# Kernel optimization log

Measured on AMD Instinct MI355X. Metric: run time of the kernel, lower is better.

The kernel has to match this reference:

```python
import jax, jax.numpy as jnp
import numpy as np

H = 50      # hidden_size (fixed in source)
IN = 7      # input_size = len(features)
B = 1024    # batch
T = 512     # seq_len
FC1 = 25
OUT = 1


def setup_inputs() -> dict:
    key = jax.random.key(0)
    ks = jax.random.split(key, 24)
    s = 1.0 / np.sqrt(H)  # PyTorch LSTM/Linear default uniform init scale

    def u(k, shape):
        return jax.random.uniform(k, shape, jnp.float32, -s, s)

    d = {"x": jax.random.normal(ks[0], (B, T, IN), jnp.float32)}
    # 4 stacked LSTM layers total: lstm1 has 2 layers (in=7 then 50), lstm2 has 2 layers (in=50)
    in_sizes = [IN, H, H, H]
    for l, isz in enumerate(in_sizes):
        d[f"Wih{l}"] = u(ks[1 + 4 * l], (4 * H, isz))
        d[f"Whh{l}"] = u(ks[2 + 4 * l], (4 * H, H))
        d[f"bih{l}"] = u(ks[3 + 4 * l], (4 * H,))
        d[f"bhh{l}"] = u(ks[4 + 4 * l], (4 * H,))
    d["W1"] = u(ks[17], (FC1, H))
    d["b1"] = u(ks[18], (FC1,))
    d["W2"] = u(ks[19], (OUT, FC1))
    d["b2"] = u(ks[20], (OUT,))
    return d


def _lstm_layer(x, Wih, Whh, bih, bhh):
    # x: [B, T, in] -> hidden sequence [B, T, H]. PyTorch gate order: i, f, g, o.
    b, t, _ = x.shape
    h = Whh.shape[1]
    # Precompute input projection for all timesteps in one big GEMM: [T, B, 4H]
    xp = jnp.einsum('bti,gi->tbg', x, Wih) + (bih + bhh)

    def step(carry, xt):
        hs, cs = carry
        gates = xt + hs @ Whh.T                      # [B, 4H]
        i, f, g, o = jnp.split(gates, 4, axis=-1)
        i = jax.nn.sigmoid(i)
        f = jax.nn.sigmoid(f)
        g = jnp.tanh(g)
        o = jax.nn.sigmoid(o)
        cs = f * cs + i * g
        hs = o * jnp.tanh(cs)
        return (hs, cs), hs

    h0 = jnp.zeros((b, h), x.dtype)
    _, hseq = jax.lax.scan(step, (h0, h0), xp)       # hseq: [T, B, H]
    return hseq.transpose(1, 0, 2)


def reference(x, Wih0, Whh0, bih0, bhh0, Wih1, Whh1, bih1, bhh1,
              Wih2, Whh2, bih2, bhh2, Wih3, Whh3, bih3, bhh3,
              W1, b1, W2, b2):
    out = x
    layers = [(Wih0, Whh0, bih0, bhh0), (Wih1, Whh1, bih1, bhh1),
              (Wih2, Whh2, bih2, bhh2), (Wih3, Whh3, bih3, bhh3)]
    for Wih, Whh, bih, bhh in layers:
        out = _lstm_layer(out, Wih, Whh, bih, bhh)
    h = out[:, -1, :]                                # last timestep [B, H]
    # dropout is identity in eval mode
    h = jax.nn.relu(h @ W1.T + b1)
    return h @ W2.T + b2                             # [B, 1]
```

## Files before the change

### kernel.cpp

```cpp
#include <hip/hip_runtime.h>


#define H 50
#define INSZ 7
#define TT 512
#define NL 4
#define FC1N 25
#define BPG 4
#define NBLK 256
#define NTHREADS 1024
#define HS 80
#define BIASL 56

typedef _Float16 half_t;
typedef __attribute__((ext_vector_type(8))) _Float16 half8_t;
typedef __attribute__((ext_vector_type(4))) float float4_t;

struct Params {
  const float* x;
  const float* Wih[NL];
  const float* Whh[NL];
  const float* bih[NL];
  const float* bhh[NL];
  const float* W1;
  const float* b1;
  const float* W2;
  const float* b2;
  float* out;
};

#define MFMA16(A, B, C) __builtin_amdgcn_mfma_f32_16x16x32_f16((A), (B), (C), 0, 0, 0)
#define EXP2F(x) __builtin_amdgcn_exp2f(x)
#define RCPF(x) __builtin_amdgcn_rcpf(x)

__global__ __launch_bounds__(NTHREADS, 4) void lstm_r8(Params p) {
  __shared__ __align__(16) half_t Xpack[2][BPG][HS];
  __shared__ __align__(16) half_t Hbuf[3][2][BPG][HS];
  __shared__ __align__(16) half_t Xstage[64][BPG][8];
  __shared__ float fc_h[BPG][H];
  __shared__ float fc1_buf[BPG][FC1N];

  const int tid = threadIdx.x;
  const int b0 = blockIdx.x * BPG;
  const int lane = tid & 63;
  const int quad = lane >> 4;
  const int col = lane & 15;
  const int glay = tid >> 8;
  const int wl = (((tid >> 6) & 3) + glay) & 3;

  half8_t afrag[4][4];
#pragma unroll
  for (int t4 = 0; t4 < 4; ++t4) {
#pragma unroll
    for (int g = 0; g < 4; ++g) {
      half8_t v;
#pragma unroll
      for (int j = 0; j < 8; ++j) {
        const int r = wl * 64 + t4 * 16 + col;
        const int u = r >> 2, q = r & 3;
        const int k = g * 32 + quad * 8 + j;
        float wv = 0.0f;
        if (u < H) {
          const int row = q * H + u;
          if (glay == 0) {
            if (k < INSZ) wv = p.Wih[0][row * INSZ + k];
            else if (k == 7) wv = p.bih[0][row] + p.bhh[0][row];
            else if (k >= 8 && k < 8 + H) wv = p.Whh[0][row * H + (k - 8)];
          } else if (glay == 1) {
            if (k == 7) wv = p.bih[1][row] + p.bhh[1][row];
            else if (k >= 8 && k < 8 + H) wv = p.Wih[1][row * H + (k - 8)];
            else if (k >= 64 && k < 64 + H) wv = p.Whh[1][row * H + (k - 64)];
          } else {
            if (k < H) wv = p.Wih[glay][row * H + k];
            else if (k == BIASL) wv = p.bih[glay][row] + p.bhh[glay][row];
            else if (k >= 64 && k < 64 + H) wv = p.Whh[glay][row * H + (k - 64)];
          }
        }
        v[j] = (half_t)wv;
      }
      afrag[t4][g] = v;
    }
  }

  {
    unsigned* xz = (unsigned*)Xpack;
    for (int i = tid; i < 2 * BPG * HS / 2; i += NTHREADS) xz[i] = 0u;
    unsigned* hz = (unsigned*)Hbuf;
    for (int i = tid; i < 3 * 2 * BPG * HS / 2; i += NTHREADS) hz[i] = 0u;
  }
  __syncthreads();
  if (tid < 8) {
    Xpack[tid >> 2][tid & 3][7] = (half_t)1.0f;
  } else if (tid < 8 + 24) {
    const int i = tid - 8, l = i >> 3, pr = (i >> 2) & 1, b = i & 3;
    Hbuf[l][pr][b][BIASL] = (half_t)1.0f;
  }
  for (int i = tid; i < 64 * BPG * INSZ; i += NTHREADS) {
    const int t = i / (BPG * INSZ), rem = i % (BPG * INSZ);
    const int b = rem / INSZ, k = rem % INSZ;
    const half_t xh = (half_t)p.x[((size_t)(b0 + b) * TT + t) * INSZ + k];
    Xstage[t][b][k] = xh;
    if (t == 0) Xpack[0][b][k] = xh;
  }
  __syncthreads();

  const int bb = col & 3;
  const int tsel = col >> 2;
  const int uu = 16 * wl + 4 * tsel + quad;
  const bool updact = (uu < H);

  const half_t* pin2[2];
  const half_t* pown2[2];
  half_t* pst2[2];
  if (glay == 0) {
    pin2[0] = &Xpack[0][bb][quad * 8];
    pin2[1] = &Xpack[1][bb][quad * 8];
    pown2[0] = pin2[0];
    pown2[1] = pin2[1];
    pst2[0] = &Xpack[1][bb][8 + uu];
    pst2[1] = &Xpack[0][bb][8 + uu];
  } else if (glay == 1) {
    pin2[0] = &Xpack[0][bb][quad * 8];
    pin2[1] = &Xpack[1][bb][quad * 8];
    pown2[0] = &Hbuf[0][0][bb][quad * 8];
    pown2[1] = &Hbuf[0][1][bb][quad * 8];
    pst2[0] = &Hbuf[0][1][bb][uu];
    pst2[1] = &Hbuf[0][0][bb][uu];
  } else {
    pin2[0] = &Hbuf[glay - 2][0][bb][quad * 8];
    pin2[1] = &Hbuf[glay - 2][1][bb][quad * 8];
    pown2[0] = &Hbuf[glay - 1][0][bb][quad * 8];
    pown2[1] = &Hbuf[glay - 1][1][bb][quad * 8];
    pst2[0] = &Hbuf[glay - 1][1][bb][uu];
    pst2[1] = &Hbuf[glay - 1][0][bb][uu];
  }
  const half_t* in_e = pin2[0];
  const half_t* in_o = pin2[1];
  const half_t* own_e = pown2[0];
  const half_t* own_o = pown2[1];
  half_t* st_e = pst2[0];
  half_t* st_o = pst2[1];

  const bool xwave = (glay == 0) && (wl == 3);
  const bool xcopy = xwave && (lane < BPG * INSZ);
  const int cb = lane / INSZ, ck = lane % INSZ;
  const int rb = lane >> 5;
  const int rt = lane & 31;

  float cst = 0.0f;
  const float4_t fzc = {0.0f, 0.0f, 0.0f, 0.0f};

#define TICK_BODY(PIN, POWN, PST, FCW)                                          \
  {                                                                             \
    float4_t a0 = fzc, a1 = fzc, a2 = fzc, a3 = fzc;                            \
    if (glay == 0) {                                                            \
      const half8_t v0 = *(const half8_t*)(PIN);                                \
      const half8_t v1 = *(const half8_t*)((PIN) + 32);                         \
      if (wl != 3) {                                                            \
        a0 = MFMA16(afrag[0][0], v0, a0); a1 = MFMA16(afrag[1][0], v0, a1);     \
        a2 = MFMA16(afrag[2][0], v0, a2); a3 = MFMA16(afrag[3][0], v0, a3);     \
        a0 = MFMA16(afrag[0][1], v1, a0); a1 = MFMA16(afrag[1][1], v1, a1);     \
        a2 = MFMA16(afrag[2][1], v1, a2); a3 = MFMA16(afrag[3][1], v1, a3);     \
      } else {                                                                  \
        a0 = MFMA16(afrag[0][0], v0, a0);                                       \
        a0 = MFMA16(afrag[0][1], v1, a0);                                       \
      }                                                                         \
    } else {                                                                    \
      const half8_t v0 = *(const half8_t*)(PIN);                                \
      const half8_t v1 = *(const half8_t*)((PIN) + 32);                         \
      const half8_t v2 = *(const half8_t*)(POWN);                               \
      const half8_t v3 = *(const half8_t*)((POWN) + 32);                        \
      if (wl != 3) {                                                            \
        a0 = MFMA16(afrag[0][0], v0, a0); a1 = MFMA16(afrag[1][0], v0, a1);     \
        a2 = MFMA16(afrag[2][0], v0, a2); a3 = MFMA16(afrag[3][0], v0, a3);     \
        a0 = MFMA16(afrag[0][1], v1, a0); a1 = MFMA16(afrag[1][1], v1, a1);     \
        a2 = MFMA16(afrag[2][1], v1, a2); a3 = MFMA16(afrag[3][1], v1, a3);     \
        a0 = MFMA16(afrag[0][2], v2, a0); a1 = MFMA16(afrag[1][2], v2, a1);     \
        a2 = MFMA16(afrag[2][2], v2, a2); a3 = MFMA16(afrag[3][2], v2, a3);     \
        a0 = MFMA16(afrag[0][3], v3, a0); a1 = MFMA16(afrag[1][3], v3, a1);     \
        a2 = MFMA16(afrag[2][3], v3, a2); a3 = MFMA16(afrag[3][3], v3, a3);     \
      } else {                                                                  \
        a0 = MFMA16(afrag[0][0], v0, a0);                                       \
        a0 = MFMA16(afrag[0][1], v1, a0);                                       \
        a0 = MFMA16(afrag[0][2], v2, a0);                                       \
        a0 = MFMA16(afrag[0][3], v3, a0);                                       \
      }                                                                         \
    }                                                                           \
    if (updact) {                                                               \
      const float4_t g01 = (col & 4) ? a1 : a0;                                 \
      const float4_t g23 = (col & 4) ? a3 : a2;                                 \
      const float4_t ga = (col & 8) ? g23 : g01;                                \
      const float di = 1.0f + EXP2F(-1.442695041f * ga[0]);                     \
      const float df = 1.0f + EXP2F(-1.442695041f * ga[1]);                     \
      const float dg = 1.0f + EXP2F(-2.885390082f * ga[2]);                     \
      const float dq = 1.0f + EXP2F(-1.442695041f * ga[3]);                     \
      const float r1 = RCPF(di * df);                                           \
      const float r2 = RCPF(dg * dq);                                           \
      const float gi = r1 * df;                                                 \
      const float gf = r1 * di;                                                 \
      const float gg = 2.0f * (r2 * dq) - 1.0f;                                 \
      const float go = r2 * dg;                                                 \
      cst = gf * cst + gi * gg;                                                 \
      const float dc = 1.0f + EXP2F(-2.885390082f * cst);                       \
      const float h = go * (2.0f * RCPF(dc) - 1.0f);                            \
      *(PST) = (half_t)h;                                                       \
      if (FCW) fc_h[bb][uu] = h;                                                \
    }                                                                           \
  }

#define XCOPY(S)                                                                \
  if (xcopy) {                                                                  \
    const int tn = (S) + 1;                                                     \
    Xpack[tn & 1][cb][ck] = Xstage[tn & 63][cb][ck];                            \
  }

  for (int s = 0; s < 3; ++s) {
    const int t = s - glay;
    if (t >= 0) {
      const int ph = s & 1;
      TICK_BODY(pin2[ph], pown2[ph], pst2[ph], false)
    }
    XCOPY(s)
    __syncthreads();
  }

  for (int s = 3; s < 511; s += 2) {
    {
      TICK_BODY(in_o, own_o, st_o, false)
      XCOPY(s)
    }
    __syncthreads();
    {
      const int s2 = s + 1;
      if (xwave && (s2 & 31) == 8 && s2 < 480) {
        const int tb = (s2 & ~31) + 32;
#pragma unroll
        for (int pp = 0; pp < 2; ++pp) {
          const int b = rb + 2 * pp;
          const int t = tb + rt;
          const float* src = &p.x[((size_t)(b0 + b) * TT + t) * INSZ];
          half_t* dst = &Xstage[t & 63][b][0];
#pragma unroll
          for (int k = 0; k < INSZ; ++k) dst[k] = (half_t)src[k];
        }
      }
      TICK_BODY(in_e, own_e, st_e, false)
      XCOPY(s2)
    }
    __syncthreads();
  }

  for (int s = 511; s < TT + NL - 1; ++s) {
    const int t = s - glay;
    if (t < TT) {
      const int ph = s & 1;
      const bool fcw = (glay == NL - 1) && (t == TT - 1);
      TICK_BODY(pin2[ph], pown2[ph], pst2[ph], fcw)
    }
    __syncthreads();
  }

  if (tid < BPG * FC1N) {
    const int b = tid / FC1N, j = tid % FC1N;
    const float* w = p.W1 + j * H;
    float a = p.b1[j];
#pragma unroll
    for (int k = 0; k < H; ++k) a += fc_h[b][k] * w[k];
    fc1_buf[b][j] = fmaxf(a, 0.0f);
  }
  __syncthreads();
  if (tid < BPG) {
    float a = p.b2[0];
#pragma unroll
    for (int j = 0; j < FC1N; ++j) a += fc1_buf[tid][j] * p.W2[j];
    p.out[b0 + tid] = a;
  }
}

extern "C" void kernel_launch(void* const* d_in, const int* in_sizes, int n_in,
                              void* d_out, int out_size, void* d_ws, size_t ws_size,
                              hipStream_t stream) {
  Params p;
  p.x = (const float*)d_in[0];
  for (int l = 0; l < NL; ++l) {
    p.Wih[l] = (const float*)d_in[1 + 4 * l];
    p.Whh[l] = (const float*)d_in[2 + 4 * l];
    p.bih[l] = (const float*)d_in[3 + 4 * l];
    p.bhh[l] = (const float*)d_in[4 + 4 * l];
  }
  p.W1 = (const float*)d_in[17];
  p.b1 = (const float*)d_in[18];
  p.W2 = (const float*)d_in[19];
  p.b2 = (const float*)d_in[20];
  p.out = (float*)d_out;

  hipLaunchKernelGGL(lstm_r8, dim3(NBLK), dim3(NTHREADS), 0, stream, p);
}
```

Baseline: 474.0 us.

## Split layer input and recurrent MFMAs across ticks to shorten the critical path

For layers above the first, the input-projection MFMAs for the next timestep now run right after the current update and accumulate into persistent registers. The following tick then only adds the recurrent contribution before the gate math. This takes half the MFMA chain off the path between each barrier and the update that depends on it. The price is a deeper layer wavefront (each layer lags by two ticks instead of one), so more prologue and epilogue ticks, plus extra live accumulator registers.

```diff
diff --git a/kernel.cpp b/kernel.cpp
--- a/kernel.cpp
+++ b/kernel.cpp
@@ -33,7 +33,7 @@
 #define EXP2F(x) __builtin_amdgcn_exp2f(x)
 #define RCPF(x) __builtin_amdgcn_rcpf(x)
 
-__global__ __launch_bounds__(NTHREADS, 4) void lstm_r8(Params p) {
+__global__ __launch_bounds__(NTHREADS, 4) void lstm_r9(Params p) {
   __shared__ __align__(16) half_t Xpack[2][BPG][HS];
   __shared__ __align__(16) half_t Hbuf[3][2][BPG][HS];
   __shared__ __align__(16) half_t Xstage[64][BPG][8];
@@ -149,62 +149,110 @@
 
   float cst = 0.0f;
   const float4_t fzc = {0.0f, 0.0f, 0.0f, 0.0f};
-
-#define TICK_BODY(PIN, POWN, PST, FCW)                                          \
+  float4_t c0 = fzc, c1 = fzc, c2 = fzc, c3 = fzc;
+
+#define UPDATE(A0, A1, A2, A3, PST, FCW)                                        \
   {                                                                             \
-    float4_t a0 = fzc, a1 = fzc, a2 = fzc, a3 = fzc;                            \
-    if (glay == 0) {                                                            \
-      const half8_t v0 = *(const half8_t*)(PIN);                                \
-      const half8_t v1 = *(const half8_t*)((PIN) + 32);                         \
-      if (wl != 3) {                                                            \
-        a0 = MFMA16(afrag[0][0], v0, a0); a1 = MFMA16(afrag[1][0], v0, a1);     \
-        a2 = MFMA16(afrag[2][0], v0, a2); a3 = MFMA16(afrag[3][0], v0, a3);     \
-        a0 = MFMA16(afrag[0][1], v1, a0); a1 = MFMA16(afrag[1][1], v1, a1);     \
-        a2 = MFMA16(afrag[2][1], v1, a2); a3 = MFMA16(afrag[3][1], v1, a3);     \
-      } else {                                                                  \
-        a0 = MFMA16(afrag[0][0], v0, a0);                                       \
-        a0 = MFMA16(afrag[0][1], v1, a0);                                       \
+    const float4_t g01 = (col & 4) ? (A1) : (A0);                               \
+    const float4_t g23 = (col & 4) ? (A3) : (A2);                               \
+    const float4_t ga = (col & 8) ? g23 : g01;                                  \
+    const float di = 1.0f + EXP2F(-1.442695041f * ga[0]);                       \
+    const float df = 1.0f + EXP2F(-1.442695041f * ga[1]);                       \
+    const float dg = 1.0f + EXP2F(-2.885390082f * ga[2]);                       \
+    const float dq = 1.0f + EXP2F(-1.442695041f * ga[3]);                       \
+    const float r1 = RCPF(di * df);                                             \
+    const float r2 = RCPF(dg * dq);                                             \
+    const float gi = r1 * df;                                                   \
+    const float gf = r1 * di;                                                   \
+    const float gg = 2.0f * (r2 * dq) - 1.0f;                                   \
+    const float go = r2 * dg;                                                   \
+    cst = gf * cst + gi * gg;                                                   \
+    const float dc = 1.0f + EXP2F(-2.885390082f * cst);                         \
+    const float h = go * (2.0f * RCPF(dc) - 1.0f);                              \
+    if (updact) {                                                               \
+      *(PST) = (half_t)h;                                                       \
+      if (FCW) fc_h[bb][uu] = h;                                                \
+    }                                                                           \
+  }
+
+#define SLOT_L0(PIN, PST, FCW)                                                  \
+  {                                                                             \
+    const half8_t v0 = *(const half8_t*)(PIN);                                  \
+    const half8_t v1 = *(const half8_t*)((PIN) + 32);                           \
+    if (wl != 3) {                                                              \
+      float4_t a0 = fzc, a1 = fzc, a2 = fzc, a3 = fzc;                          \
+      a0 = MFMA16(afrag[0][0], v0, a0); a1 = MFMA16(afrag[1][0], v0, a1);       \
+      a2 = MFMA16(afrag[2][0], v0, a2); a3 = MFMA16(afrag[3][0], v0, a3);       \
+      a0 = MFMA16(afrag[0][1], v1, a0); a1 = MFMA16(afrag[1][1], v1, a1);       \
+      a2 = MFMA16(afrag[2][1], v1, a2); a3 = MFMA16(afrag[3][1], v1, a3);       \
+      UPDATE(a0, a1, a2, a3, PST, FCW)                                          \
+    } else {                                                                    \
+      float4_t a0 = fzc;                                                        \
+      a0 = MFMA16(afrag[0][0], v0, a0);                                         \
+      a0 = MFMA16(afrag[0][1], v1, a0);                                         \
+      UPDATE(a0, a0, a0, a0, PST, FCW)                                          \
+    }                                                                           \
+  }
+
+#define SLOT_LX(PIN, POWN, PST, FCW)                                            \
+  {                                                                             \
+    const half8_t v2 = *(const half8_t*)(POWN);                                 \
+    const half8_t v3 = *(const half8_t*)((POWN) + 32);                          \
+    const half8_t u0 = *(const half8_t*)(PIN);                                  \
+    const half8_t u1 = *(const half8_t*)((PIN) + 32);                           \
+    if (wl != 3) {                                                              \
+      c0 = MFMA16(afrag[0][2], v2, c0); c1 = MFMA16(afrag[1][2], v2, c1);       \
+      c2 = MFMA16(afrag[2][2], v2, c2); c3 = MFMA16(afrag[3][2], v2, c3);       \
+      c0 = MFMA16(afrag[0][3], v3, c0); c1 = MFMA16(afrag[1][3], v3, c1);       \
+      c2 = MFMA16(afrag[2][3], v3, c2); c3 = MFMA16(afrag[3][3], v3, c3);       \
+      UPDATE(c0, c1, c2, c3, PST, FCW)                                          \
+      c0 = MFMA16(afrag[0][0], u0, fzc); c1 = MFMA16(afrag[1][0], u0, fzc);     \
+      c2 = MFMA16(afrag[2][0], u0, fzc); c3 = MFMA16(afrag[3][0], u0, fzc);     \
+      c0 = MFMA16(afrag[0][1], u1, c0); c1 = MFMA16(afrag[1][1], u1, c1);       \
+      c2 = MFMA16(afrag[2][1], u1, c2); c3 = MFMA16(afrag[3][1], u1, c3);       \
+    } else {                                                                    \
+      c0 = MFMA16(afrag[0][2], v2, c0);                                         \
+      c0 = MFMA16(afrag[0][3], v3, c0);                                         \
+      UPDATE(c0, c0, c0, c0, PST, FCW)                                          \
+      c0 = MFMA16(afrag[0][0], u0, fzc);                                        \
+      c0 = MFMA16(afrag[0][1], u1, c0);                                         \
+    }                                                                           \
+  }
+
+#define SLOT_LX_G(PIN, POWN, PST, DOOWN, DOIN, FCW)                             \
+  {                                                                             \
+    if (wl != 3) {                                                              \
+      if (DOOWN) {                                                              \
+        const half8_t v2 = *(const half8_t*)(POWN);                             \
+        const half8_t v3 = *(const half8_t*)((POWN) + 32);                      \
+        c0 = MFMA16(afrag[0][2], v2, c0); c1 = MFMA16(afrag[1][2], v2, c1);     \
+        c2 = MFMA16(afrag[2][2], v2, c2); c3 = MFMA16(afrag[3][2], v2, c3);     \
+        c0 = MFMA16(afrag[0][3], v3, c0); c1 = MFMA16(afrag[1][3], v3, c1);     \
+        c2 = MFMA16(afrag[2][3], v3, c2); c3 = MFMA16(afrag[3][3], v3, c3);     \
+        UPDATE(c0, c1, c2, c3, PST, FCW)                                        \
+      }                                                                         \
+      if (DOIN) {                                                               \
+        const half8_t u0 = *(const half8_t*)(PIN);                              \
+        const half8_t u1 = *(const half8_t*)((PIN) + 32);                       \
+        c0 = MFMA16(afrag[0][0], u0, fzc); c1 = MFMA16(afrag[1][0], u0, fzc);   \
+        c2 = MFMA16(afrag[2][0], u0, fzc); c3 = MFMA16(afrag[3][0], u0, fzc);   \
+        c0 = MFMA16(afrag[0][1], u1, c0); c1 = MFMA16(afrag[1][1], u1, c1);     \
+        c2 = MFMA16(afrag[2][1], u1, c2); c3 = MFMA16(afrag[3][1], u1, c3);     \
       }                                                                         \
     } else {                                                                    \
-      const half8_t v0 = *(const half8_t*)(PIN);                                \
-      const half8_t v1 = *(const half8_t*)((PIN) + 32);                         \
-      const half8_t v2 = *(const half8_t*)(POWN);                               \
-      const half8_t v3 = *(const half8_t*)((POWN) + 32);                        \
-      if (wl != 3) {                                                            \
-        a0 = MFMA16(afrag[0][0], v0, a0); a1 = MFMA16(afrag[1][0], v0, a1);     \
-        a2 = MFMA16(afrag[2][0], v0, a2); a3 = MFMA16(afrag[3][0], v0, a3);     \
-        a0 = MFMA16(afrag[0][1], v1, a0); a1 = MFMA16(afrag[1][1], v1, a1);     \
-        a2 = MFMA16(afrag[2][1], v1, a2); a3 = MFMA16(afrag[3][1], v1, a3);     \
-        a0 = MFMA16(afrag[0][2], v2, a0); a1 = MFMA16(afrag[1][2], v2, a1);     \
-        a2 = MFMA16(afrag[2][2], v2, a2); a3 = MFMA16(afrag[3][2], v2, a3);     \
-        a0 = MFMA16(afrag[0][3], v3, a0); a1 = MFMA16(afrag[1][3], v3, a1);     \
-        a2 = MFMA16(afrag[2][3], v3, a2); a3 = MFMA16(afrag[3][3], v3, a3);     \
-      } else {                                                                  \
-        a0 = MFMA16(afrag[0][0], v0, a0);                                       \
-        a0 = MFMA16(afrag[0][1], v1, a0);                                       \
-        a0 = MFMA16(afrag[0][2], v2, a0);                                       \
-        a0 = MFMA16(afrag[0][3], v3, a0);                                       \
+      if (DOOWN) {                                                              \
+        const half8_t v2 = *(const half8_t*)(POWN);                             \
+        const half8_t v3 = *(const half8_t*)((POWN) + 32);                      \
+        c0 = MFMA16(afrag[0][2], v2, c0);                                       \
+        c0 = MFMA16(afrag[0][3], v3, c0);                                       \
+        UPDATE(c0, c0, c0, c0, PST, FCW)                                        \
       }                                                                         \
-    }                                                                           \
-    if (updact) {                                                               \
-      const float4_t g01 = (col & 4) ? a1 : a0;                                 \
-      const float4_t g23 = (col & 4) ? a3 : a2;                                 \
-      const float4_t ga = (col & 8) ? g23 : g01;                                \
-      const float di = 1.0f + EXP2F(-1.442695041f * ga[0]);                     \
-      const float df = 1.0f + EXP2F(-1.442695041f * ga[1]);                     \
-      const float dg = 1.0f + EXP2F(-2.885390082f * ga[2]);                     \
-      const float dq = 1.0f + EXP2F(-1.442695041f * ga[3]);                     \
-      const float r1 = RCPF(di * df);                                           \
-      const float r2 = RCPF(dg * dq);                                           \
-      const float gi = r1 * df;                                                 \
-      const float gf = r1 * di;                                                 \
-      const float gg = 2.0f * (r2 * dq) - 1.0f;                                 \
-      const float go = r2 * dg;                                                 \
-      cst = gf * cst + gi * gg;                                                 \
-      const float dc = 1.0f + EXP2F(-2.885390082f * cst);                       \
-      const float h = go * (2.0f * RCPF(dc) - 1.0f);                            \
-      *(PST) = (half_t)h;                                                       \
-      if (FCW) fc_h[bb][uu] = h;                                                \
+      if (DOIN) {                                                               \
+        const half8_t u0 = *(const half8_t*)(PIN);                              \
+        const half8_t u1 = *(const half8_t*)((PIN) + 32);                       \
+        c0 = MFMA16(afrag[0][0], u0, fzc);                                      \
+        c0 = MFMA16(afrag[0][1], u1, c0);                                       \
+      }                                                                         \
     }                                                                           \
   }
 
@@ -214,26 +262,22 @@
     Xpack[tn & 1][cb][ck] = Xstage[tn & 63][cb][ck];                            \
   }
 
-  for (int s = 0; s < 3; ++s) {
-    const int t = s - glay;
-    if (t >= 0) {
-      const int ph = s & 1;
-      TICK_BODY(pin2[ph], pown2[ph], pst2[ph], false)
+  for (int s = 0; s < 6; ++s) {
+    const int ph = s & 1;
+    if (glay == 0) {
+      SLOT_L0(pin2[ph], pst2[ph], false)
+    } else {
+      SLOT_LX_G(pin2[ph], pown2[ph], pst2[ph], s >= 2 * glay, s >= 2 * glay - 1,
+                false)
     }
     XCOPY(s)
     __syncthreads();
   }
 
-  for (int s = 3; s < 511; s += 2) {
+  for (int s = 6; s < 512; s += 2) {
     {
-      TICK_BODY(in_o, own_o, st_o, false)
-      XCOPY(s)
-    }
-    __syncthreads();
-    {
-      const int s2 = s + 1;
-      if (xwave && (s2 & 31) == 8 && s2 < 480) {
-        const int tb = (s2 & ~31) + 32;
+      if (xwave && (s & 31) == 8 && s < 480) {
+        const int tb = (s & ~31) + 32;
 #pragma unroll
         for (int pp = 0; pp < 2; ++pp) {
           const int b = rb + 2 * pp;
@@ -244,18 +288,31 @@
           for (int k = 0; k < INSZ; ++k) dst[k] = (half_t)src[k];
         }
       }
-      TICK_BODY(in_e, own_e, st_e, false)
-      XCOPY(s2)
+      if (glay == 0) {
+        SLOT_L0(in_e, st_e, false)
+      } else {
+        SLOT_LX(in_e, own_e, st_e, false)
+      }
+      XCOPY(s)
     }
     __syncthreads();
-  }
-
-  for (int s = 511; s < TT + NL - 1; ++s) {
-    const int t = s - glay;
-    if (t < TT) {
-      const int ph = s & 1;
+    {
+      if (glay == 0) {
+        SLOT_L0(in_o, st_o, false)
+      } else {
+        SLOT_LX(in_o, own_o, st_o, false)
+      }
+      XCOPY(s + 1)
+    }
+    __syncthreads();
+  }
+
+  for (int s = 512; s < TT + 2 * (NL - 1); ++s) {
+    const int ph = s & 1;
+    if (glay > 0) {
+      const int t = s - 2 * glay;
       const bool fcw = (glay == NL - 1) && (t == TT - 1);
-      TICK_BODY(pin2[ph], pown2[ph], pst2[ph], fcw)
+      SLOT_LX_G(pin2[ph], pown2[ph], pst2[ph], t < TT, t + 1 < TT, fcw)
     }
     __syncthreads();
   }
@@ -294,5 +351,5 @@
   p.b2 = (const float*)d_in[20];
   p.out = (float*)d_out;
 
-  hipLaunchKernelGGL(lstm_r8, dim3(NBLK), dim3(NTHREADS), 0, stream, p);
+  hipLaunchKernelGGL(lstm_r9, dim3(NBLK), dim3(NTHREADS), 0, stream, p);
 }
```

Result: slower. 523.2 us (+10.4%).

## Split LSTM into input-projection and recurrent waves with pipelined preactivation buffers

Applied to the files above, without the earlier changes.

Each layer now gets two waves. One computes the input projection plus bias a step ahead into a double-buffered fp32 preactivation buffer, and the other does only the Whh recurrence and gate update. This shortens the per-step critical path, since the recurrent wave runs just two MFMA K-chunks per unit group. The block drops to 512 threads, and layers are staggered by two steps, so the pipeline lengthens. Gate scaling constants are folded into the weights. Register pressure rises because each wave holds 13x2 weight fragments and 13 accumulators, and the final-layer hidden state for the FC head is read back in fp16.

```diff
diff --git a/kernel.cpp b/kernel.cpp
--- a/kernel.cpp
+++ b/kernel.cpp
@@ -8,9 +8,12 @@
 #define FC1N 25
 #define BPG 4
 #define NBLK 256
-#define NTHREADS 1024
-#define HS 80
-#define BIASL 56
+#define NTHREADS 512
+#define NCH 13
+#define HRS 80
+#define PRS 216
+#define XD 32
+#define XW 32
 
 typedef _Float16 half_t;
 typedef __attribute__((ext_vector_type(8))) _Float16 half8_t;
@@ -33,11 +36,25 @@
 #define EXP2F(x) __builtin_amdgcn_exp2f(x)
 #define RCPF(x) __builtin_amdgcn_rcpf(x)
 
-__global__ __launch_bounds__(NTHREADS, 4) void lstm_r8(Params p) {
-  __shared__ __align__(16) half_t Xpack[2][BPG][HS];
-  __shared__ __align__(16) half_t Hbuf[3][2][BPG][HS];
-  __shared__ __align__(16) half_t Xstage[64][BPG][8];
-  __shared__ float fc_h[BPG][H];
+#define UPD(g, c, h)                                                     \
+  const float di = 1.0f + EXP2F((g)[0]);                                 \
+  const float df = 1.0f + EXP2F((g)[1]);                                 \
+  const float dgg = 1.0f + EXP2F((g)[2]);                                \
+  const float dq = 1.0f + EXP2F((g)[3]);                                 \
+  const float r1 = RCPF(di * df);                                        \
+  const float r2 = RCPF(dgg * dq);                                       \
+  const float gi = r1 * df;                                              \
+  const float gf = r1 * di;                                              \
+  const float gg = 2.0f * (r2 * dq) - 1.0f;                              \
+  const float go = r2 * dgg;                                             \
+  (c) = gf * (c) + gi * gg;                                              \
+  const float dc = 1.0f + EXP2F(-2.885390082f * (c));                    \
+  const float h = go * (2.0f * RCPF(dc) - 1.0f);
+
+__global__ __launch_bounds__(NTHREADS, 2) void lstm_r11(Params p) {
+  __shared__ __align__(16) half_t hring[NL][8][BPG][HRS];
+  __shared__ __align__(16) half_t xring[XD][BPG][XW];
+  __shared__ __align__(16) float preb[NL][2][BPG][PRS];
   __shared__ float fc1_buf[BPG][FC1N];
 
   const int tid = threadIdx.x;
@@ -45,227 +62,145 @@
   const int lane = tid & 63;
   const int quad = lane >> 4;
   const int col = lane & 15;
-  const int glay = tid >> 8;
-  const int wl = (((tid >> 6) & 3) + glay) & 3;
-
-  half8_t afrag[4][4];
-#pragma unroll
-  for (int t4 = 0; t4 < 4; ++t4) {
-#pragma unroll
-    for (int g = 0; g < 4; ++g) {
-      half8_t v;
-#pragma unroll
-      for (int j = 0; j < 8; ++j) {
-        const int r = wl * 64 + t4 * 16 + col;
-        const int u = r >> 2, q = r & 3;
-        const int k = g * 32 + quad * 8 + j;
-        float wv = 0.0f;
-        if (u < H) {
-          const int row = q * H + u;
-          if (glay == 0) {
-            if (k < INSZ) wv = p.Wih[0][row * INSZ + k];
-            else if (k == 7) wv = p.bih[0][row] + p.bhh[0][row];
-            else if (k >= 8 && k < 8 + H) wv = p.Whh[0][row * H + (k - 8)];
-          } else if (glay == 1) {
-            if (k == 7) wv = p.bih[1][row] + p.bhh[1][row];
-            else if (k >= 8 && k < 8 + H) wv = p.Wih[1][row * H + (k - 8)];
-            else if (k >= 64 && k < 64 + H) wv = p.Whh[1][row * H + (k - 64)];
-          } else {
-            if (k < H) wv = p.Wih[glay][row * H + k];
-            else if (k == BIASL) wv = p.bih[glay][row] + p.bhh[glay][row];
-            else if (k >= 64 && k < 64 + H) wv = p.Whh[glay][row * H + (k - 64)];
+  const int w = tid >> 6;
+  const bool isrec = (w < 4);
+  const int lay = w & 3;
+  const int bb = col & 3;
+  const int tsel = col >> 2;
+
+  half8_t af[NCH][2];
+  {
+    const int q = col & 3;
+#pragma unroll
+    for (int cc = 0; cc < NCH; ++cc) {
+      const int u = cc * 4 + tsel;
+#pragma unroll
+      for (int kg = 0; kg < 2; ++kg) {
+        half8_t v;
+#pragma unroll
+        for (int j = 0; j < 8; ++j) {
+          const int k = kg * 32 + quad * 8 + j;
+          float wv = 0.0f;
+          if (u < H) {
+            const int row = q * H + u;
+            if (isrec) {
+              if (k < H) wv = p.Whh[lay][row * H + k];
+            } else if (lay == 0) {
+              if (k < INSZ) wv = p.Wih[0][row * INSZ + k];
+              else if (k == INSZ) wv = p.bih[0][row] + p.bhh[0][row];
+            } else {
+              if (k < H) wv = p.Wih[lay][row * H + k];
+              else if (k == H) wv = p.bih[lay][row] + p.bhh[lay][row];
+            }
+            wv *= (q == 2) ? -2.885390082f : -1.442695041f;
           }
-        }
-        v[j] = (half_t)wv;
+          v[j] = (half_t)wv;
+        }
+        af[cc][kg] = v;
       }
-      afrag[t4][g] = v;
     }
   }
 
   {
-    unsigned* xz = (unsigned*)Xpack;
-    for (int i = tid; i < 2 * BPG * HS / 2; i += NTHREADS) xz[i] = 0u;
-    unsigned* hz = (unsigned*)Hbuf;
-    for (int i = tid; i < 3 * 2 * BPG * HS / 2; i += NTHREADS) hz[i] = 0u;
+    unsigned* hz = (unsigned*)hring;
+    for (int i = tid; i < (int)(NL * 8 * BPG * HRS / 2); i += NTHREADS) hz[i] = 0u;
+    unsigned* xz = (unsigned*)xring;
+    for (int i = tid; i < (int)(XD * BPG * XW / 2); i += NTHREADS) xz[i] = 0u;
   }
   __syncthreads();
-  if (tid < 8) {
-    Xpack[tid >> 2][tid & 3][7] = (half_t)1.0f;
-  } else if (tid < 8 + 24) {
-    const int i = tid - 8, l = i >> 3, pr = (i >> 2) & 1, b = i & 3;
-    Hbuf[l][pr][b][BIASL] = (half_t)1.0f;
-  }
-  for (int i = tid; i < 64 * BPG * INSZ; i += NTHREADS) {
+  for (int i = tid; i < NL * 8 * BPG; i += NTHREADS) {
+    const int l = i >> 5, sl = (i >> 2) & 7, b = i & 3;
+    hring[l][sl][b][H] = (half_t)1.0f;
+  }
+  for (int i = tid; i < XD * BPG; i += NTHREADS) {
+    xring[i >> 2][i & 3][INSZ] = (half_t)1.0f;
+  }
+  for (int i = tid; i < XD * BPG * INSZ; i += NTHREADS) {
     const int t = i / (BPG * INSZ), rem = i % (BPG * INSZ);
     const int b = rem / INSZ, k = rem % INSZ;
-    const half_t xh = (half_t)p.x[((size_t)(b0 + b) * TT + t) * INSZ + k];
-    Xstage[t][b][k] = xh;
-    if (t == 0) Xpack[0][b][k] = xh;
+    xring[t][b][k] = (half_t)p.x[((size_t)(b0 + b) * TT + t) * INSZ + k];
   }
   __syncthreads();
 
-  const int bb = col & 3;
-  const int tsel = col >> 2;
-  const int uu = 16 * wl + 4 * tsel + quad;
-  const bool updact = (uu < H);
-
-  const half_t* pin2[2];
-  const half_t* pown2[2];
-  half_t* pst2[2];
-  if (glay == 0) {
-    pin2[0] = &Xpack[0][bb][quad * 8];
-    pin2[1] = &Xpack[1][bb][quad * 8];
-    pown2[0] = pin2[0];
-    pown2[1] = pin2[1];
-    pst2[0] = &Xpack[1][bb][8 + uu];
-    pst2[1] = &Xpack[0][bb][8 + uu];
-  } else if (glay == 1) {
-    pin2[0] = &Xpack[0][bb][quad * 8];
-    pin2[1] = &Xpack[1][bb][quad * 8];
-    pown2[0] = &Hbuf[0][0][bb][quad * 8];
-    pown2[1] = &Hbuf[0][1][bb][quad * 8];
-    pst2[0] = &Hbuf[0][1][bb][uu];
-    pst2[1] = &Hbuf[0][0][bb][uu];
-  } else {
-    pin2[0] = &Hbuf[glay - 2][0][bb][quad * 8];
-    pin2[1] = &Hbuf[glay - 2][1][bb][quad * 8];
-    pown2[0] = &Hbuf[glay - 1][0][bb][quad * 8];
-    pown2[1] = &Hbuf[glay - 1][1][bb][quad * 8];
-    pst2[0] = &Hbuf[glay - 1][1][bb][uu];
-    pst2[1] = &Hbuf[glay - 1][0][bb][uu];
-  }
-  const half_t* in_e = pin2[0];
-  const half_t* in_o = pin2[1];
-  const half_t* own_e = pown2[0];
-  const half_t* own_o = pown2[1];
-  half_t* st_e = pst2[0];
-  half_t* st_o = pst2[1];
-
-  const bool xwave = (glay == 0) && (wl == 3);
-  const bool xcopy = xwave && (lane < BPG * INSZ);
-  const int cb = lane / INSZ, ck = lane % INSZ;
-  const int rb = lane >> 5;
-  const int rt = lane & 31;
-
-  float cst = 0.0f;
-  const float4_t fzc = {0.0f, 0.0f, 0.0f, 0.0f};
-
-#define TICK_BODY(PIN, POWN, PST, FCW)                                          \
-  {                                                                             \
-    float4_t a0 = fzc, a1 = fzc, a2 = fzc, a3 = fzc;                            \
-    if (glay == 0) {                                                            \
-      const half8_t v0 = *(const half8_t*)(PIN);                                \
-      const half8_t v1 = *(const half8_t*)((PIN) + 32);                         \
-      if (wl != 3) {                                                            \
-        a0 = MFMA16(afrag[0][0], v0, a0); a1 = MFMA16(afrag[1][0], v0, a1);     \
-        a2 = MFMA16(afrag[2][0], v0, a2); a3 = MFMA16(afrag[3][0], v0, a3);     \
-        a0 = MFMA16(afrag[0][1], v1, a0); a1 = MFMA16(afrag[1][1], v1, a1);     \
-        a2 = MFMA16(afrag[2][1], v1, a2); a3 = MFMA16(afrag[3][1], v1, a3);     \
-      } else {                                                                  \
-        a0 = MFMA16(afrag[0][0], v0, a0);                                       \
-        a0 = MFMA16(afrag[0][1], v1, a0);                                       \
-      }                                                                         \
-    } else {                                                                    \
-      const half8_t v0 = *(const half8_t*)(PIN);                                \
-      const half8_t v1 = *(const half8_t*)((PIN) + 32);                         \
-      const half8_t v2 = *(const half8_t*)(POWN);                               \
-      const half8_t v3 = *(const half8_t*)((POWN) + 32);                        \
-      if (wl != 3) {                                                            \
-        a0 = MFMA16(afrag[0][0], v0, a0); a1 = MFMA16(afrag[1][0], v0, a1);     \
-        a2 = MFMA16(afrag[2][0], v0, a2); a3 = MFMA16(afrag[3][0], v0, a3);     \
-        a0 = MFMA16(afrag[0][1], v1, a0); a1 = MFMA16(afrag[1][1], v1, a1);     \
-        a2 = MFMA16(afrag[2][1], v1, a2); a3 = MFMA16(afrag[3][1], v1, a3);     \
-        a0 = MFMA16(afrag[0][2], v2, a0); a1 = MFMA16(afrag[1][2], v2, a1);     \
-        a2 = MFMA16(afrag[2][2], v2, a2); a3 = MFMA16(afrag[3][2], v2, a3);     \
-        a0 = MFMA16(afrag[0][3], v3, a0); a1 = MFMA16(afrag[1][3], v3, a1);     \
-        a2 = MFMA16(afrag[2][3], v3, a2); a3 = MFMA16(afrag[3][3], v3, a3);     \
-      } else {                                                                  \
-        a0 = MFMA16(afrag[0][0], v0, a0);                                       \
-        a0 = MFMA16(afrag[0][1], v1, a0);                                       \
-        a0 = MFMA16(afrag[0][2], v2, a0);                                       \
-        a0 = MFMA16(afrag[0][3], v3, a0);                                       \
-      }                                                                         \
-    }                                                                           \
-    if (updact) {                                                               \
-      const float4_t g01 = (col & 4) ? a1 : a0;                                 \
-      const float4_t g23 = (col & 4) ? a3 : a2;                                 \
-      const float4_t ga = (col & 8) ? g23 : g01;                                \
-      const float di = 1.0f + EXP2F(-1.442695041f * ga[0]);                     \
-      const float df = 1.0f + EXP2F(-1.442695041f * ga[1]);                     \
-      const float dg = 1.0f + EXP2F(-2.885390082f * ga[2]);                     \
-      const float dq = 1.0f + EXP2F(-1.442695041f * ga[3]);                     \
-      const float r1 = RCPF(di * df);                                           \
-      const float r2 = RCPF(dg * dq);                                           \
-      const float gi = r1 * df;                                                 \
-      const float gf = r1 * di;                                                 \
-      const float gg = 2.0f * (r2 * dq) - 1.0f;                                 \
-      const float go = r2 * dg;                                                 \
-      cst = gf * cst + gi * gg;                                                 \
-      const float dc = 1.0f + EXP2F(-2.885390082f * cst);                       \
-      const float h = go * (2.0f * RCPF(dc) - 1.0f);                            \
-      *(PST) = (half_t)h;                                                       \
-      if (FCW) fc_h[bb][uu] = h;                                                \
-    }                                                                           \
-  }
-
-#define XCOPY(S)                                                                \
-  if (xcopy) {                                                                  \
-    const int tn = (S) + 1;                                                     \
-    Xpack[tn & 1][cb][ck] = Xstage[tn & 63][cb][ck];                            \
-  }
-
-  for (int s = 0; s < 3; ++s) {
-    const int t = s - glay;
-    if (t >= 0) {
-      const int ph = s & 1;
-      TICK_BODY(pin2[ph], pown2[ph], pst2[ph], false)
-    }
-    XCOPY(s)
-    __syncthreads();
-  }
-
-  for (int s = 3; s < 511; s += 2) {
-    {
-      TICK_BODY(in_o, own_o, st_o, false)
-      XCOPY(s)
+  float csts[4] = {0.0f, 0.0f, 0.0f, 0.0f};
+  const float4_t fz = {0.0f, 0.0f, 0.0f, 0.0f};
+
+  const int NSTEP = TT + 2 * NL - 1;
+  for (int s = 0; s < NSTEP; ++s) {
+    if (isrec) {
+      const int t = s - 2 * lay - 1;
+      if ((unsigned)t < TT) {
+        float4_t acc[NCH];
+        const half_t* hb = &hring[lay][(t - 1) & 7][bb][quad * 8];
+        const half8_t v0 = *(const half8_t*)(hb);
+        const half8_t v1 = *(const half8_t*)(hb + 32);
+        const float* pp = &preb[lay][s & 1][bb][quad * 4];
+#pragma unroll
+        for (int cc = 0; cc < NCH; ++cc)
+          acc[cc] = *(const float4_t*)(pp + cc * 16);
+#pragma unroll
+        for (int cc = 0; cc < NCH; ++cc) acc[cc] = MFMA16(af[cc][0], v0, acc[cc]);
+#pragma unroll
+        for (int cc = 0; cc < NCH; ++cc) acc[cc] = MFMA16(af[cc][1], v1, acc[cc]);
+        half_t* hw = &hring[lay][t & 7][bb][0];
+#pragma unroll
+        for (int j = 0; j < 3; ++j) {
+          const float4_t va = (tsel & 1) ? acc[4 * j + 1] : acc[4 * j + 0];
+          const float4_t vb = (tsel & 1) ? acc[4 * j + 3] : acc[4 * j + 2];
+          const float4_t ga = (tsel & 2) ? vb : va;
+          UPD(ga, csts[j], h)
+          hw[4 * tsel + 16 * j + quad] = (half_t)h;
+        }
+        {
+          const float4_t ga = acc[12];
+          UPD(ga, csts[3], h)
+          if (tsel == 0 && quad < 2) hw[48 + quad] = (half_t)h;
+        }
+      }
+    } else {
+      const int t2 = s - 2 * lay;
+      if ((unsigned)t2 < TT) {
+        if (lay == 0 && (s & 15) == 0 && s + 16 < TT) {
+          const int t0 = s + 16 + (lane >> 2);
+          const int rb = lane & 3;
+          if (t0 < TT) {
+            const float* src = &p.x[((size_t)(b0 + rb) * TT + t0) * INSZ];
+            half_t* dst = &xring[t0 & 31][rb][0];
+#pragma unroll
+            for (int k = 0; k < INSZ; ++k) dst[k] = (half_t)src[k];
+          }
+        }
+        float4_t acc[NCH];
+        const half_t* hb = (lay == 0)
+                               ? &xring[t2 & 31][bb][quad * 8]
+                               : &hring[lay - 1][t2 & 7][bb][quad * 8];
+        const half8_t v0 = *(const half8_t*)(hb);
+#pragma unroll
+        for (int cc = 0; cc < NCH; ++cc) acc[cc] = MFMA16(af[cc][0], v0, fz);
+        if (lay != 0) {
+          const half8_t v1 = *(const half8_t*)(hb + 32);
+#pragma unroll
+          for (int cc = 0; cc < NCH; ++cc)
+            acc[cc] = MFMA16(af[cc][1], v1, acc[cc]);
+        }
+        if (tsel == 0) {
+          float* pw = &preb[lay][(s + 1) & 1][bb][quad * 4];
+#pragma unroll
+          for (int cc = 0; cc < NCH; ++cc)
+            *(float4_t*)(pw + cc * 16) = acc[cc];
+        }
+      }
     }
     __syncthreads();
-    {
-      const int s2 = s + 1;
-      if (xwave && (s2 & 31) == 8 && s2 < 480) {
-        const int tb = (s2 & ~31) + 32;
-#pragma unroll
-        for (int pp = 0; pp < 2; ++pp) {
-          const int b = rb + 2 * pp;
-          const int t = tb + rt;
-          const float* src = &p.x[((size_t)(b0 + b) * TT + t) * INSZ];
-          half_t* dst = &Xstage[t & 63][b][0];
-#pragma unroll
-          for (int k = 0; k < INSZ; ++k) dst[k] = (half_t)src[k];
-        }
-      }
-      TICK_BODY(in_e, own_e, st_e, false)
-      XCOPY(s2)
-    }
-    __syncthreads();
-  }
-
-  for (int s = 511; s < TT + NL - 1; ++s) {
-    const int t = s - glay;
-    if (t < TT) {
-      const int ph = s & 1;
-      const bool fcw = (glay == NL - 1) && (t == TT - 1);
-      TICK_BODY(pin2[ph], pown2[ph], pst2[ph], fcw)
-    }
-    __syncthreads();
   }
 
   if (tid < BPG * FC1N) {
     const int b = tid / FC1N, j = tid % FC1N;
-    const float* w = p.W1 + j * H;
+    const float* wgt = p.W1 + j * H;
     float a = p.b1[j];
 #pragma unroll
-    for (int k = 0; k < H; ++k) a += fc_h[b][k] * w[k];
+    for (int k = 0; k < H; ++k)
+      a += (float)hring[3][(TT - 1) & 7][b][k] * wgt[k];
     fc1_buf[b][j] = fmaxf(a, 0.0f);
   }
   __syncthreads();
@@ -294,5 +229,5 @@
   p.b2 = (const float*)d_in[20];
   p.out = (float*)d_out;
 
-  hipLaunchKernelGGL(lstm_r8, dim3(NBLK), dim3(NTHREADS), 0, stream, p);
+  hipLaunchKernelGGL(lstm_r11, dim3(NBLK), dim3(NTHREADS), 0, stream, p);
 }
```

After: 1.305 ms. 2.75x slower.
